# Kernel optimization log

Hardware: AMD Instinct MI355X
Metric: run time of the kernel (lower is better)

The kernel has to match this reference:

```python
import jax, jax.numpy as jnp
import numpy as np
import math

DIM = 512
HEADS = 8
DIM_HEAD = 64
INNER = HEADS * DIM_HEAD


def setup_inputs() -> dict:
    key = jax.random.key(0)
    k1, k2, k3, k4 = jax.random.split(key, 4)
    x = jax.random.normal(k1, (8, 1024, DIM), dtype=jnp.float32)
    w_qkv = jax.random.normal(k2, (DIM, INNER * 3), dtype=jnp.float32) / math.sqrt(DIM)
    w_out = jax.random.normal(k3, (INNER, DIM), dtype=jnp.float32) / math.sqrt(INNER)
    temperature = jnp.array(math.log(DIM_HEAD ** -0.5), dtype=jnp.float32)
    return {"x": x, "w_qkv": w_qkv, "w_out": w_out, "temperature": temperature}


def reference(x, w_qkv, w_out, temperature):
    b, n, _ = x.shape
    qkv = x @ w_qkv  # [b, n, 3*inner]
    q, k, v = jnp.split(qkv, 3, axis=-1)
    # [b, n, h*d] -> [b, h, n, d]
    def split_heads(t):
        return t.reshape(b, n, HEADS, DIM_HEAD).transpose(0, 2, 1, 3)
    q, k, v = split_heads(q), split_heads(k), split_heads(v)
    dots = jnp.einsum('bhnd,bhmd->bhnm', q, k) * jnp.exp(temperature)
    mask_value = -jnp.finfo(dots.dtype).max
    eye = jnp.eye(n, dtype=bool)
    dots = jnp.where(eye, mask_value, dots)
    attn = jax.nn.softmax(dots, axis=-1)
    out = jnp.einsum('bhnm,bhmd->bhnd', attn, v)
    out = out.transpose(0, 2, 1, 3).reshape(b, n, INNER)
    return out @ w_out
```

## Files before the change

### kernel.cpp

```cpp
#include <hip/hip_runtime.h>
#include <math.h>

#define BATCH  8
#define SEQ    1024
#define DMODEL 512
#define NHEADS 8
#define DHEAD  64
#define MTOT   (BATCH*SEQ)
#define QKVLD  (3*DMODEL)

typedef unsigned short ushortT;
typedef __attribute__((ext_vector_type(8))) short short8;
typedef __attribute__((ext_vector_type(4))) float f32x4;

typedef __attribute__((address_space(3))) unsigned char lds_byte;
typedef __attribute__((address_space(1))) const unsigned char glob_byte;

__device__ inline void g2l16(const void* g, void* l) {
    __builtin_amdgcn_global_load_lds((glob_byte*)g, (lds_byte*)l, 16, 0, 0);
}

__device__ inline ushortT f2bf(float f) {
    union { float f; unsigned u; } v; v.f = f;
    unsigned r = (v.u + 0x7FFFu + ((v.u >> 16) & 1u)) >> 16;
    return (ushortT)r;
}
__device__ inline ushortT f2bf_fast(float f) {
    union { float f; unsigned u; } v; v.f = f;
    return (ushortT)((v.u + 0x8000u) >> 16);
}

__global__ __launch_bounds__(256)
void cvt_bf16(const float* __restrict__ in, ushortT* __restrict__ out, int n8)
{
    int gid = blockIdx.x * 256 + threadIdx.x;
    if (gid >= n8) return;
    const float4 a = *(const float4*)(in + (long)gid*8);
    const float4 b = *(const float4*)(in + (long)gid*8 + 4);
    ushortT o[8];
    o[0]=f2bf(a.x); o[1]=f2bf(a.y); o[2]=f2bf(a.z); o[3]=f2bf(a.w);
    o[4]=f2bf(b.x); o[5]=f2bf(b.y); o[6]=f2bf(b.z); o[7]=f2bf(b.w);
    *(short8*)(out + (long)gid*8) = *(short8*)o;
}

__global__ __launch_bounds__(256)
void cvt_transpose(const float* __restrict__ W, ushortT* __restrict__ WT,
                   int K, int N)
{
    __shared__ float T[32][33];
    const int t = threadIdx.x;
    const int n0 = blockIdx.x * 32;
    const int k0 = blockIdx.y * 32;
    {
        const int r = t >> 3, c4 = (t & 7) * 4;
        const float4 v = *(const float4*)(W + (long)(k0 + r)*N + n0 + c4);
        T[c4+0][r] = v.x; T[c4+1][r] = v.y; T[c4+2][r] = v.z; T[c4+3][r] = v.w;
    }
    __syncthreads();
    {
        const int n = t >> 3, k4 = (t & 7) * 4;
        ushortT o[4];
        o[0] = f2bf(T[n][k4+0]); o[1] = f2bf(T[n][k4+1]);
        o[2] = f2bf(T[n][k4+2]); o[3] = f2bf(T[n][k4+3]);
        *(uint2*)(WT + (long)(n0 + n)*K + k0 + k4) = *(uint2*)o;
    }
}

template <int MODE>
__global__ __launch_bounds__(256, 3)
void gemm_bf16(const ushortT* __restrict__ A, const ushortT* __restrict__ BT,
               void* __restrict__ Cv, ushortT* __restrict__ vT,
               const float* __restrict__ temp, int M, int N, int K)
{
    __shared__ ushortT As[128*64];
    __shared__ ushortT Bs[128*64];

    const int t    = threadIdx.x;
    const int lane = t & 63;
    const int w    = t >> 6;
    const int l15  = lane & 15, l4 = lane >> 4;

    const int nwg = gridDim.x * gridDim.y;
    const int bid = blockIdx.y * gridDim.x + blockIdx.x;
    const int swz = (bid & 7) * (nwg >> 3) + (bid >> 3);
    const int bm  = swz / gridDim.x;
    const int bn  = swz % gridDim.x;

    const int srow = t >> 3;
    const int slot = t & 7;

    f32x4 acc[4][4] = {};

    for (int kt = 0; kt < K; kt += 64) {
#pragma unroll
        for (int c = 0; c < 4; ++c) {
            const int row  = c*32 + srow;
            const int scol = ((slot ^ (row & 7)) << 4);
            g2l16((const char*)(A  + (long)(bm*128 + row)*K + kt) + scol,
                  (char*)As + c*4096 + t*16);
            g2l16((const char*)(BT + (long)(bn*128 + row)*K + kt) + scol,
                  (char*)Bs + c*4096 + t*16);
        }
        asm volatile("s_waitcnt vmcnt(0)" ::: "memory");
        __syncthreads();

#pragma unroll
        for (int kk = 0; kk < 2; ++kk) {
            short8 a[4], b[4];
#pragma unroll
            for (int i = 0; i < 4; ++i) {
                const int ra = (w >> 1)*64 + i*16 + l15;
                const int ca = (kk*32 + l4*8) ^ ((ra & 7) << 3);
                a[i] = *(const short8*)&As[ra*64 + ca];
                const int rb = (w & 1)*64 + i*16 + l15;
                const int cb = (kk*32 + l4*8) ^ ((rb & 7) << 3);
                b[i] = *(const short8*)&Bs[rb*64 + cb];
            }
#pragma unroll
            for (int i = 0; i < 4; ++i)
#pragma unroll
                for (int j = 0; j < 4; ++j)
                    acc[i][j] = __builtin_amdgcn_mfma_f32_16x16x32_bf16(
                                    a[i], b[j], acc[i][j], 0, 0, 0);
        }
        __syncthreads();
    }

    if (MODE == 1 && bn >= 8) {
#pragma unroll
        for (int i = 0; i < 4; ++i) {
            const int row0 = bm*128 + (w >> 1)*64 + i*16 + l4*4;
            const int bb   = row0 >> 10, n = row0 & 1023;
#pragma unroll
            for (int j = 0; j < 4; ++j) {
                const int cg = bn*128 + (w & 1)*64 + j*16 + l15 - 1024;
                const int h = cg >> 6, d = cg & 63;
                union { ushortT u[4]; uint2 q; } pk;
#pragma unroll
                for (int r = 0; r < 4; ++r) pk.u[r] = f2bf(acc[i][j][r]);
                *(uint2*)&vT[((long)((bb*8 + h)*64 + d))*1024 + n] = pk.q;
            }
        }
        return;
    }

    const float qs = (MODE == 1) ? __expf(temp[0]) * 1.44269504f : 1.0f;
    const float mulv = (MODE == 1 && bn < 4) ? qs : 1.0f;

#pragma unroll
    for (int i = 0; i < 4; ++i) {
        const int row0 = bm*128 + (w >> 1)*64 + i*16 + l4*4;
#pragma unroll
        for (int j = 0; j < 4; ++j) {
            const int col = bn*128 + (w & 1)*64 + j*16 + l15;
#pragma unroll
            for (int r = 0; r < 4; ++r) {
                const float v = acc[i][j][r] * mulv;
                if (MODE == 1) ((ushortT*)Cv)[(long)(row0 + r)*N + col] = f2bf(v);
                else           ((float*)Cv)[(long)(row0 + r)*N + col]   = v;
            }
        }
    }
}

__global__ __launch_bounds__(256, 4)
void attn_mfma(const ushortT* __restrict__ qkv, const ushortT* __restrict__ vT,
               ushortT* __restrict__ aout)
{
    __shared__ ushortT Ps[64*64];
    __shared__ ushortT Ks[2][64*64];
    __shared__ ushortT Vs[2][64*64];

    const int t    = threadIdx.x;
    const int lane = t & 63;
    const int w    = t >> 6;
    const int l15  = lane & 15, l4 = lane >> 4;
    const int bh   = blockIdx.x;
    const int qb   = blockIdx.y;
    const int b    = bh >> 3, h = bh & 7;

    const long row0 = (long)b * SEQ * QKVLD;
    const char* vtb = (const char*)(vT + (long)bh * 64 * 1024);

    short8 onesf;
#pragma unroll
    for (int e = 0; e < 8; ++e) onesf[e] = (short)0x3F80;

    {
        const char* qbase = (const char*)(qkv + row0 + (long)qb*64*QKVLD + h*DHEAD);
        const char* kbase = (const char*)(qkv + row0 + DMODEL + h*DHEAD);
#pragma unroll
        for (int c = 0; c < 2; ++c) {
            const int row  = c*32 + (t >> 3);
            const int scol = ((t & 7) ^ (row & 7)) << 4;
            g2l16(qbase + (long)row*(QKVLD*2) + scol, (char*)Ps + c*4096 + t*16);
            g2l16(kbase + (long)row*(QKVLD*2) + scol, (char*)&Ks[0][0] + c*4096 + t*16);
            g2l16(vtb + (long)row*2048 + scol,        (char*)&Vs[0][0] + c*4096 + t*16);
        }
        asm volatile("s_waitcnt vmcnt(0)" ::: "memory");
        __syncthreads();
    }

    short8 qa[2];
#pragma unroll
    for (int kk = 0; kk < 2; ++kk) {
        const int r = w*16 + l15;
        const int c = (kk*32 + l4*8) ^ ((r & 7) << 3);
        qa[kk] = *(const short8*)&Ps[r*64 + c];
    }

    f32x4 o_[4] = {};
    f32x4 lacc  = {};

    for (int jt = 0; jt < 16; ++jt) {
        const int cur = jt & 1, nxt = cur ^ 1;
        const bool pf = (jt + 1) < 16;

        if (pf) {
            const char* kbase = (const char*)(qkv + row0 + (long)(jt+1)*64*QKVLD
                                              + DMODEL + h*DHEAD);
#pragma unroll
            for (int c = 0; c < 2; ++c) {
                const int row  = c*32 + (t >> 3);
                const int scol = ((t & 7) ^ (row & 7)) << 4;
                g2l16(kbase + (long)row*(QKVLD*2) + scol,
                      (char*)&Ks[nxt][0] + c*4096 + t*16);
                g2l16(vtb + (long)row*2048 + (jt+1)*128 + scol,
                      (char*)&Vs[nxt][0] + c*4096 + t*16);
            }
        }

        f32x4 s_[4] = {};
#pragma unroll
        for (int kk = 0; kk < 2; ++kk) {
            short8 kb[4];
#pragma unroll
            for (int j = 0; j < 4; ++j) {
                const int r = j*16 + l15;
                const int c = (kk*32 + l4*8) ^ ((r & 7) << 3);
                kb[j] = *(const short8*)&Ks[cur][r*64 + c];
            }
#pragma unroll
            for (int j = 0; j < 4; ++j)
                s_[j] = __builtin_amdgcn_mfma_f32_16x16x32_bf16(
                            qa[kk], kb[j], s_[j], 0, 0, 0);
        }

        if (jt == qb) {
#pragma unroll
            for (int r = 0; r < 4; ++r) {
                const int lrow = w*16 + l4*4 + r;
#pragma unroll
                for (int j = 0; j < 4; ++j) {
                    float p = exp2f(s_[j][r]);
                    if (j*16 + l15 == lrow) p = 0.f;
                    Ps[lrow*64 + ((j*16 + l15) ^ ((lrow & 7) << 3))] = f2bf_fast(p);
                }
            }
        } else {
#pragma unroll
            for (int r = 0; r < 4; ++r) {
                const int lrow = w*16 + l4*4 + r;
#pragma unroll
                for (int j = 0; j < 4; ++j) {
                    const float p = exp2f(s_[j][r]);
                    Ps[lrow*64 + ((j*16 + l15) ^ ((lrow & 7) << 3))] = f2bf_fast(p);
                }
            }
        }

#pragma unroll
        for (int kk = 0; kk < 2; ++kk) {
            const int rp = w*16 + l15;
            const int cp = (kk*32 + l4*8) ^ ((rp & 7) << 3);
            const short8 pa = *(const short8*)&Ps[rp*64 + cp];
            lacc = __builtin_amdgcn_mfma_f32_16x16x32_bf16(pa, onesf, lacc, 0, 0, 0);
            short8 vb[4];
#pragma unroll
            for (int j = 0; j < 4; ++j) {
                const int r = j*16 + l15;
                const int c = (kk*32 + l4*8) ^ ((r & 7) << 3);
                vb[j] = *(const short8*)&Vs[cur][r*64 + c];
            }
#pragma unroll
            for (int j = 0; j < 4; ++j)
                o_[j] = __builtin_amdgcn_mfma_f32_16x16x32_bf16(
                            pa, vb[j], o_[j], 0, 0, 0);
        }

        if (pf) asm volatile("s_waitcnt vmcnt(0)" ::: "memory");
        __syncthreads();
    }

#pragma unroll
    for (int r = 0; r < 4; ++r) {
        const float inv  = 1.0f / lacc[r];
        const long  grow = (long)b*SEQ + qb*64 + w*16 + l4*4 + r;
#pragma unroll
        for (int j = 0; j < 4; ++j)
            aout[grow*DMODEL + h*DHEAD + j*16 + l15] = f2bf(o_[j][r] * inv);
    }
}

extern "C" void kernel_launch(void* const* d_in, const int* in_sizes, int n_in,
                              void* d_out, int out_size, void* d_ws, size_t ws_size,
                              hipStream_t stream)
{
    const float* x     = (const float*)d_in[0];
    const float* w_qkv = (const float*)d_in[1];
    const float* w_out = (const float*)d_in[2];
    const float* temp  = (const float*)d_in[3];
    float* out = (float*)d_out;

    char* ws = (char*)d_ws;
    ushortT* x_bf   = (ushortT*)(ws);
    ushortT* wqkvT  = (ushortT*)(ws + 8388608);
    ushortT* woutT  = (ushortT*)(ws + 9961472);
    ushortT* qkv_bf = (ushortT*)(ws + 10485760);
    ushortT* vT     = (ushortT*)(ws + 35651584);
    ushortT* aout   = (ushortT*)(ws + 44040192);

    cvt_bf16<<<dim3((MTOT*DMODEL/8)/256), 256, 0, stream>>>(x, x_bf, MTOT*DMODEL/8);
    cvt_transpose<<<dim3(QKVLD/32, DMODEL/32), 256, 0, stream>>>(w_qkv, wqkvT, DMODEL, QKVLD);
    cvt_transpose<<<dim3(DMODEL/32, DMODEL/32), 256, 0, stream>>>(w_out, woutT, DMODEL, DMODEL);

    gemm_bf16<1><<<dim3(QKVLD/128, MTOT/128), 256, 0, stream>>>(
        x_bf, wqkvT, qkv_bf, vT, temp, MTOT, QKVLD, DMODEL);

    attn_mfma<<<dim3(BATCH*NHEADS, SEQ/64), 256, 0, stream>>>(qkv_bf, vT, aout);

    gemm_bf16<0><<<dim3(DMODEL/128, MTOT/128), 256, 0, stream>>>(
        aout, woutT, out, nullptr, nullptr, MTOT, DMODEL, DMODEL);
}
```

Measured before the change: 146.0 us.

## Double attention query tile to 128 rows and merge weight transpose launches

The attention kernel now processes 128 query rows per block, with each wave handling 32 rows, so every K/V tile loaded into LDS is reused across twice as many queries. This halves total K/V global traffic and block count, at the cost of more registers, larger LDS for P, and lower occupancy (launch bounds 4 to 3) with only 512 blocks. The diagonal mask logic is adjusted for the larger tile. Separately, the two weight convert-transpose kernels are merged into one launch to save launch overhead.

```diff
diff --git a/kernel.cpp b/kernel.cpp
--- a/kernel.cpp
+++ b/kernel.cpp
@@ -44,13 +44,16 @@
 }
 
 __global__ __launch_bounds__(256)
-void cvt_transpose(const float* __restrict__ W, ushortT* __restrict__ WT,
-                   int K, int N)
+void cvt_transpose2(const float* __restrict__ Wq, ushortT* __restrict__ WqT,
+                    const float* __restrict__ Wo, ushortT* __restrict__ WoT)
 {
     __shared__ float T[32][33];
     const int t = threadIdx.x;
-    const int n0 = blockIdx.x * 32;
-    const int k0 = blockIdx.y * 32;
+    int bid = blockIdx.x;
+    const float* W; ushortT* WT; int N, n0, k0;
+    if (bid < 768) { W = Wq; WT = WqT; N = QKVLD;  n0 = (bid % 48) * 32; k0 = (bid / 48) * 32; }
+    else { bid -= 768; W = Wo; WT = WoT; N = DMODEL; n0 = (bid % 16) * 32; k0 = (bid / 16) * 32; }
+    const int K = DMODEL;
     {
         const int r = t >> 3, c4 = (t & 7) * 4;
         const float4 v = *(const float4*)(W + (long)(k0 + r)*N + n0 + c4);
@@ -163,11 +166,11 @@
     }
 }
 
-__global__ __launch_bounds__(256, 4)
+__global__ __launch_bounds__(256, 3)
 void attn_mfma(const ushortT* __restrict__ qkv, const ushortT* __restrict__ vT,
                ushortT* __restrict__ aout)
 {
-    __shared__ ushortT Ps[64*64];
+    __shared__ ushortT Ps[128*64];
     __shared__ ushortT Ks[2][64*64];
     __shared__ ushortT Vs[2][64*64];
 
@@ -187,13 +190,18 @@
     for (int e = 0; e < 8; ++e) onesf[e] = (short)0x3F80;
 
     {
-        const char* qbase = (const char*)(qkv + row0 + (long)qb*64*QKVLD + h*DHEAD);
+        const char* qbase = (const char*)(qkv + row0 + (long)qb*128*QKVLD + h*DHEAD);
         const char* kbase = (const char*)(qkv + row0 + DMODEL + h*DHEAD);
+#pragma unroll
+        for (int c = 0; c < 4; ++c) {
+            const int row  = c*32 + (t >> 3);
+            const int scol = ((t & 7) ^ (row & 7)) << 4;
+            g2l16(qbase + (long)row*(QKVLD*2) + scol, (char*)Ps + c*4096 + t*16);
+        }
 #pragma unroll
         for (int c = 0; c < 2; ++c) {
             const int row  = c*32 + (t >> 3);
             const int scol = ((t & 7) ^ (row & 7)) << 4;
-            g2l16(qbase + (long)row*(QKVLD*2) + scol, (char*)Ps + c*4096 + t*16);
             g2l16(kbase + (long)row*(QKVLD*2) + scol, (char*)&Ks[0][0] + c*4096 + t*16);
             g2l16(vtb + (long)row*2048 + scol,        (char*)&Vs[0][0] + c*4096 + t*16);
         }
@@ -201,16 +209,18 @@
         __syncthreads();
     }
 
-    short8 qa[2];
+    short8 qa[2][2];
+#pragma unroll
+    for (int i = 0; i < 2; ++i)
 #pragma unroll
     for (int kk = 0; kk < 2; ++kk) {
-        const int r = w*16 + l15;
+        const int r = w*32 + i*16 + l15;
         const int c = (kk*32 + l4*8) ^ ((r & 7) << 3);
-        qa[kk] = *(const short8*)&Ps[r*64 + c];
-    }
-
-    f32x4 o_[4] = {};
-    f32x4 lacc  = {};
+        qa[i][kk] = *(const short8*)&Ps[r*64 + c];
+    }
+
+    f32x4 o_[2][4] = {};
+    f32x4 lacc[2]  = {};
 
     for (int jt = 0; jt < 16; ++jt) {
         const int cur = jt & 1, nxt = cur ^ 1;
@@ -230,7 +240,7 @@
             }
         }
 
-        f32x4 s_[4] = {};
+        f32x4 s_[2][4] = {};
 #pragma unroll
         for (int kk = 0; kk < 2; ++kk) {
             short8 kb[4];
@@ -241,29 +251,36 @@
                 kb[j] = *(const short8*)&Ks[cur][r*64 + c];
             }
 #pragma unroll
+            for (int i = 0; i < 2; ++i)
+#pragma unroll
             for (int j = 0; j < 4; ++j)
-                s_[j] = __builtin_amdgcn_mfma_f32_16x16x32_bf16(
-                            qa[kk], kb[j], s_[j], 0, 0, 0);
-        }
-
-        if (jt == qb) {
+                s_[i][j] = __builtin_amdgcn_mfma_f32_16x16x32_bf16(
+                               qa[i][kk], kb[j], s_[i][j], 0, 0, 0);
+        }
+
+        if ((jt >> 1) == qb) {
+            const int coff = (jt & 1) << 6;
+#pragma unroll
+            for (int i = 0; i < 2; ++i)
 #pragma unroll
             for (int r = 0; r < 4; ++r) {
-                const int lrow = w*16 + l4*4 + r;
+                const int lrow = w*32 + i*16 + l4*4 + r;
 #pragma unroll
                 for (int j = 0; j < 4; ++j) {
-                    float p = exp2f(s_[j][r]);
-                    if (j*16 + l15 == lrow) p = 0.f;
+                    float p = exp2f(s_[i][j][r]);
+                    if (coff + j*16 + l15 == lrow) p = 0.f;
                     Ps[lrow*64 + ((j*16 + l15) ^ ((lrow & 7) << 3))] = f2bf_fast(p);
                 }
             }
         } else {
 #pragma unroll
+            for (int i = 0; i < 2; ++i)
+#pragma unroll
             for (int r = 0; r < 4; ++r) {
-                const int lrow = w*16 + l4*4 + r;
+                const int lrow = w*32 + i*16 + l4*4 + r;
 #pragma unroll
                 for (int j = 0; j < 4; ++j) {
-                    const float p = exp2f(s_[j][r]);
+                    const float p = exp2f(s_[i][j][r]);
                     Ps[lrow*64 + ((j*16 + l15) ^ ((lrow & 7) << 3))] = f2bf_fast(p);
                 }
             }
@@ -271,10 +288,15 @@
 
 #pragma unroll
         for (int kk = 0; kk < 2; ++kk) {
-            const int rp = w*16 + l15;
-            const int cp = (kk*32 + l4*8) ^ ((rp & 7) << 3);
-            const short8 pa = *(const short8*)&Ps[rp*64 + cp];
-            lacc = __builtin_amdgcn_mfma_f32_16x16x32_bf16(pa, onesf, lacc, 0, 0, 0);
+            short8 pa[2];
+#pragma unroll
+            for (int i = 0; i < 2; ++i) {
+                const int rp = w*32 + i*16 + l15;
+                const int cp = (kk*32 + l4*8) ^ ((rp & 7) << 3);
+                pa[i] = *(const short8*)&Ps[rp*64 + cp];
+                lacc[i] = __builtin_amdgcn_mfma_f32_16x16x32_bf16(
+                              pa[i], onesf, lacc[i], 0, 0, 0);
+            }
             short8 vb[4];
 #pragma unroll
             for (int j = 0; j < 4; ++j) {
@@ -283,9 +305,11 @@
                 vb[j] = *(const short8*)&Vs[cur][r*64 + c];
             }
 #pragma unroll
+            for (int i = 0; i < 2; ++i)
+#pragma unroll
             for (int j = 0; j < 4; ++j)
-                o_[j] = __builtin_amdgcn_mfma_f32_16x16x32_bf16(
-                            pa, vb[j], o_[j], 0, 0, 0);
+                o_[i][j] = __builtin_amdgcn_mfma_f32_16x16x32_bf16(
+                               pa[i], vb[j], o_[i][j], 0, 0, 0);
         }
 
         if (pf) asm volatile("s_waitcnt vmcnt(0)" ::: "memory");
@@ -293,12 +317,14 @@
     }
 
 #pragma unroll
+    for (int i = 0; i < 2; ++i)
+#pragma unroll
     for (int r = 0; r < 4; ++r) {
-        const float inv  = 1.0f / lacc[r];
-        const long  grow = (long)b*SEQ + qb*64 + w*16 + l4*4 + r;
+        const float inv  = 1.0f / lacc[i][r];
+        const long  grow = (long)b*SEQ + qb*128 + w*32 + i*16 + l4*4 + r;
 #pragma unroll
         for (int j = 0; j < 4; ++j)
-            aout[grow*DMODEL + h*DHEAD + j*16 + l15] = f2bf(o_[j][r] * inv);
+            aout[grow*DMODEL + h*DHEAD + j*16 + l15] = f2bf(o_[i][j][r] * inv);
     }
 }
 
@@ -321,13 +347,12 @@
     ushortT* aout   = (ushortT*)(ws + 44040192);
 
     cvt_bf16<<<dim3((MTOT*DMODEL/8)/256), 256, 0, stream>>>(x, x_bf, MTOT*DMODEL/8);
-    cvt_transpose<<<dim3(QKVLD/32, DMODEL/32), 256, 0, stream>>>(w_qkv, wqkvT, DMODEL, QKVLD);
-    cvt_transpose<<<dim3(DMODEL/32, DMODEL/32), 256, 0, stream>>>(w_out, woutT, DMODEL, DMODEL);
+    cvt_transpose2<<<dim3(1024), 256, 0, stream>>>(w_qkv, wqkvT, w_out, woutT);
 
     gemm_bf16<1><<<dim3(QKVLD/128, MTOT/128), 256, 0, stream>>>(
         x_bf, wqkvT, qkv_bf, vT, temp, MTOT, QKVLD, DMODEL);
 
-    attn_mfma<<<dim3(BATCH*NHEADS, SEQ/64), 256, 0, stream>>>(qkv_bf, vT, aout);
+    attn_mfma<<<dim3(BATCH*NHEADS, SEQ/128), 256, 0, stream>>>(qkv_bf, vT, aout);
 
     gemm_bf16<0><<<dim3(DMODEL/128, MTOT/128), 256, 0, stream>>>(
         aout, woutT, out, nullptr, nullptr, MTOT, DMODEL, DMODEL);
```

Result: faster. 141.0 us (-3.4%).

## Double attention query tile to 128 rows and fuse conversion kernels

Applied to the files above, without the earlier changes.

The attention kernel now handles 128 query rows per block with 512 threads (eight waves). Each staged K/V tile is shared by twice as many waves, which halves redundant K/V global loads, and the diagonal mask is adjusted for the larger query block. The three input/weight conversion kernels are merged into one launch to save launch overhead. The trade-offs are half as many attention blocks to spread across the CUs and a launch bound of 512×4 that may squeeze the register budget.

```diff
diff --git a/kernel.cpp b/kernel.cpp
--- a/kernel.cpp
+++ b/kernel.cpp
@@ -31,26 +31,28 @@
 }
 
 __global__ __launch_bounds__(256)
-void cvt_bf16(const float* __restrict__ in, ushortT* __restrict__ out, int n8)
-{
-    int gid = blockIdx.x * 256 + threadIdx.x;
-    if (gid >= n8) return;
-    const float4 a = *(const float4*)(in + (long)gid*8);
-    const float4 b = *(const float4*)(in + (long)gid*8 + 4);
-    ushortT o[8];
-    o[0]=f2bf(a.x); o[1]=f2bf(a.y); o[2]=f2bf(a.z); o[3]=f2bf(a.w);
-    o[4]=f2bf(b.x); o[5]=f2bf(b.y); o[6]=f2bf(b.z); o[7]=f2bf(b.w);
-    *(short8*)(out + (long)gid*8) = *(short8*)o;
-}
-
-__global__ __launch_bounds__(256)
-void cvt_transpose(const float* __restrict__ W, ushortT* __restrict__ WT,
-                   int K, int N)
+void cvt_all(const float* __restrict__ x, ushortT* __restrict__ x_bf,
+             const float* __restrict__ Wq, ushortT* __restrict__ WqT,
+             const float* __restrict__ Wo, ushortT* __restrict__ WoT)
 {
     __shared__ float T[32][33];
     const int t = threadIdx.x;
-    const int n0 = blockIdx.x * 32;
-    const int k0 = blockIdx.y * 32;
+    int bid = blockIdx.x;
+    if (bid < 2048) {
+        const int gid = bid * 256 + t;
+        const float4 a = *(const float4*)(x + (long)gid*8);
+        const float4 b = *(const float4*)(x + (long)gid*8 + 4);
+        ushortT o[8];
+        o[0]=f2bf(a.x); o[1]=f2bf(a.y); o[2]=f2bf(a.z); o[3]=f2bf(a.w);
+        o[4]=f2bf(b.x); o[5]=f2bf(b.y); o[6]=f2bf(b.z); o[7]=f2bf(b.w);
+        *(short8*)(x_bf + (long)gid*8) = *(short8*)o;
+        return;
+    }
+    bid -= 2048;
+    const float* W; ushortT* WT; int N, n0, k0;
+    if (bid < 768) { W = Wq; WT = WqT; N = QKVLD;  n0 = (bid % 48) * 32; k0 = (bid / 48) * 32; }
+    else { bid -= 768; W = Wo; WT = WoT; N = DMODEL; n0 = (bid % 16) * 32; k0 = (bid / 16) * 32; }
+    const int K = DMODEL;
     {
         const int r = t >> 3, c4 = (t & 7) * 4;
         const float4 v = *(const float4*)(W + (long)(k0 + r)*N + n0 + c4);
@@ -163,11 +165,11 @@
     }
 }
 
-__global__ __launch_bounds__(256, 4)
+__global__ __launch_bounds__(512, 4)
 void attn_mfma(const ushortT* __restrict__ qkv, const ushortT* __restrict__ vT,
                ushortT* __restrict__ aout)
 {
-    __shared__ ushortT Ps[64*64];
+    __shared__ ushortT Ps[128*64];
     __shared__ ushortT Ks[2][64*64];
     __shared__ ushortT Vs[2][64*64];
 
@@ -187,15 +189,20 @@
     for (int e = 0; e < 8; ++e) onesf[e] = (short)0x3F80;
 
     {
-        const char* qbase = (const char*)(qkv + row0 + (long)qb*64*QKVLD + h*DHEAD);
+        const char* qbase = (const char*)(qkv + row0 + (long)qb*128*QKVLD + h*DHEAD);
         const char* kbase = (const char*)(qkv + row0 + DMODEL + h*DHEAD);
 #pragma unroll
         for (int c = 0; c < 2; ++c) {
-            const int row  = c*32 + (t >> 3);
+            const int idx  = c*512 + t;
+            const int row  = idx >> 3;
+            const int scol = ((idx & 7) ^ (row & 7)) << 4;
+            g2l16(qbase + (long)row*(QKVLD*2) + scol, (char*)Ps + c*8192 + t*16);
+        }
+        {
+            const int row  = t >> 3;
             const int scol = ((t & 7) ^ (row & 7)) << 4;
-            g2l16(qbase + (long)row*(QKVLD*2) + scol, (char*)Ps + c*4096 + t*16);
-            g2l16(kbase + (long)row*(QKVLD*2) + scol, (char*)&Ks[0][0] + c*4096 + t*16);
-            g2l16(vtb + (long)row*2048 + scol,        (char*)&Vs[0][0] + c*4096 + t*16);
+            g2l16(kbase + (long)row*(QKVLD*2) + scol, (char*)&Ks[0][0] + t*16);
+            g2l16(vtb + (long)row*2048 + scol,        (char*)&Vs[0][0] + t*16);
         }
         asm volatile("s_waitcnt vmcnt(0)" ::: "memory");
         __syncthreads();
@@ -219,15 +226,10 @@
         if (pf) {
             const char* kbase = (const char*)(qkv + row0 + (long)(jt+1)*64*QKVLD
                                               + DMODEL + h*DHEAD);
-#pragma unroll
-            for (int c = 0; c < 2; ++c) {
-                const int row  = c*32 + (t >> 3);
-                const int scol = ((t & 7) ^ (row & 7)) << 4;
-                g2l16(kbase + (long)row*(QKVLD*2) + scol,
-                      (char*)&Ks[nxt][0] + c*4096 + t*16);
-                g2l16(vtb + (long)row*2048 + (jt+1)*128 + scol,
-                      (char*)&Vs[nxt][0] + c*4096 + t*16);
-            }
+            const int row  = t >> 3;
+            const int scol = ((t & 7) ^ (row & 7)) << 4;
+            g2l16(kbase + (long)row*(QKVLD*2) + scol, (char*)&Ks[nxt][0] + t*16);
+            g2l16(vtb + (long)row*2048 + (jt+1)*128 + scol, (char*)&Vs[nxt][0] + t*16);
         }
 
         f32x4 s_[4] = {};
@@ -246,14 +248,15 @@
                             qa[kk], kb[j], s_[j], 0, 0, 0);
         }
 
-        if (jt == qb) {
+        if ((jt >> 1) == qb) {
+            const int coff = (jt & 1) << 6;
 #pragma unroll
             for (int r = 0; r < 4; ++r) {
                 const int lrow = w*16 + l4*4 + r;
 #pragma unroll
                 for (int j = 0; j < 4; ++j) {
                     float p = exp2f(s_[j][r]);
-                    if (j*16 + l15 == lrow) p = 0.f;
+                    if (coff + j*16 + l15 == lrow) p = 0.f;
                     Ps[lrow*64 + ((j*16 + l15) ^ ((lrow & 7) << 3))] = f2bf_fast(p);
                 }
             }
@@ -295,7 +298,7 @@
 #pragma unroll
     for (int r = 0; r < 4; ++r) {
         const float inv  = 1.0f / lacc[r];
-        const long  grow = (long)b*SEQ + qb*64 + w*16 + l4*4 + r;
+        const long  grow = (long)b*SEQ + qb*128 + w*16 + l4*4 + r;
 #pragma unroll
         for (int j = 0; j < 4; ++j)
             aout[grow*DMODEL + h*DHEAD + j*16 + l15] = f2bf(o_[j][r] * inv);
@@ -320,14 +323,12 @@
     ushortT* vT     = (ushortT*)(ws + 35651584);
     ushortT* aout   = (ushortT*)(ws + 44040192);
 
-    cvt_bf16<<<dim3((MTOT*DMODEL/8)/256), 256, 0, stream>>>(x, x_bf, MTOT*DMODEL/8);
-    cvt_transpose<<<dim3(QKVLD/32, DMODEL/32), 256, 0, stream>>>(w_qkv, wqkvT, DMODEL, QKVLD);
-    cvt_transpose<<<dim3(DMODEL/32, DMODEL/32), 256, 0, stream>>>(w_out, woutT, DMODEL, DMODEL);
+    cvt_all<<<dim3(3072), 256, 0, stream>>>(x, x_bf, w_qkv, wqkvT, w_out, woutT);
 
     gemm_bf16<1><<<dim3(QKVLD/128, MTOT/128), 256, 0, stream>>>(
         x_bf, wqkvT, qkv_bf, vT, temp, MTOT, QKVLD, DMODEL);
 
-    attn_mfma<<<dim3(BATCH*NHEADS, SEQ/64), 256, 0, stream>>>(qkv_bf, vT, aout);
+    attn_mfma<<<dim3(BATCH*NHEADS, SEQ/128), 512, 0, stream>>>(qkv_bf, vT, aout);
 
     gemm_bf16<0><<<dim3(DMODEL/128, MTOT/128), 256, 0, stream>>>(
         aout, woutT, out, nullptr, nullptr, MTOT, DMODEL, DMODEL);
```

Result: faster. 135.5 us (-7.2%).
